# Performance work log

Measured on AMD Instinct MI355X. Metric: run time of the kernel, lower is better.

The kernel has to match this reference:

```python
import jax, jax.numpy as jnp
import numpy as np

E, N, LAT = 200000, 50000, 128
EPS = 1e-8

def _split(x):
    # irreps layout 64x0e | 32x1e | 16x2e, mul-major: [E,64], [E,32,3], [E,16,5]
    n = x.shape[0]
    return x[:, :64], x[:, 64:160].reshape(n, 32, 3), x[:, 160:240].reshape(n, 16, 5)

def _merge(x0, x1, x2):
    n = x0.shape[0]
    return jnp.concatenate([x0, x1.reshape(n, -1), x2.reshape(n, -1)], axis=-1)

def _sep_ln(x, w0, b0, w1, w2):
    # separable layer norm: standard LN on l=0 scalars, degree-balanced RMS on l>0
    x0, x1, x2 = _split(x)
    x0c = x0 - x0.mean(-1, keepdims=True)
    y0 = x0c * jax.lax.rsqrt((x0c * x0c).mean(-1, keepdims=True) + EPS) * w0 + b0
    var = 0.5 * ((x1 * x1).mean((-2, -1)) + (x2 * x2).mean((-2, -1)))
    inv = jax.lax.rsqrt(var + EPS)[:, None, None]
    return _merge(y0, x1 * inv * w1[None, :, None], x2 * inv * w2[None, :, None])

def _rot(x0, x1, x2, D, back=False):
    # per-l Wigner-D block rotation; D is block-diag [E,9,9] (l=0:1x1, l=1:3x3, l=2:5x5)
    sub = 'eji,ecj->eci' if back else 'eij,ecj->eci'
    y0 = x0 * D[:, 0, 0][:, None]
    y1 = jnp.einsum(sub, D[:, 1:4, 1:4], x1)
    y2 = jnp.einsum(sub, D[:, 4:9, 4:9], x2)
    return y0, y1, y2

def _silu(x):
    return x * jax.nn.sigmoid(x)

def _forward(latents, node_features, edge_features, edge_vector, wigner_D_all,
             ln_n_w0, ln_n_b0, ln_n_w1, ln_n_w2, ln_e_w0, ln_e_b0, ln_e_w1, ln_e_w2,
             so2_w0, so2_w1r, so2_w1i, so2_w2r, so2_w2i, lp_w0, lp_b0, lp_w1, lp_w2,
             edge_index, active_edges):
    nn = _sep_ln(node_features, ln_n_w0, ln_n_b0, ln_n_w1, ln_n_w2)
    ne = _sep_ln(edge_features, ln_e_w0, ln_e_b0, ln_e_w1, ln_e_w2)
    ec = edge_index[0][active_edges]
    en = edge_index[1][active_edges]
    lat = latents[active_edges]
    D = wigner_D_all
    # rotate each segment (center | edge | neighbor) into the edge frame (tp_rotate_in)
    segs = [_rot(*_split(s), D) for s in (nn[ec], ne, nn[en])]
    # group by SO(2) order m (index within (2l+1) components is l+m)
    m0 = jnp.concatenate([jnp.concatenate([s0, s1[:, :, 1], s2[:, :, 2]], -1) for s0, s1, s2 in segs] + [lat], -1)  # [E,464]
    p1 = jnp.concatenate([jnp.concatenate([s1[:, :, 2], s2[:, :, 3]], -1) for _, s1, s2 in segs], -1)  # [E,144]
    n1 = jnp.concatenate([jnp.concatenate([s1[:, :, 0], s2[:, :, 1]], -1) for _, s1, s2 in segs], -1)
    p2 = jnp.concatenate([s2[:, :, 4] for _, _, s2 in segs], -1)  # [E,48]
    n2 = jnp.concatenate([s2[:, :, 0] for _, _, s2 in segs], -1)
    # SO(2) linear: real map for m=0 (latents injected), complex 2x2 maps for m>0
    o0 = (m0 @ so2_w0) * (1.0 / np.sqrt(464.0))  # [E,160] = 112 scalars+gates | 32 l1-m0 | 16 l2-m0
    inv1 = 1.0 / np.sqrt(144.0)
    op1 = (p1 @ so2_w1r - n1 @ so2_w1i) * inv1
    on1 = (p1 @ so2_w1i + n1 @ so2_w1r) * inv1
    inv2 = 1.0 / np.sqrt(48.0)
    op2 = (p2 @ so2_w2r - n2 @ so2_w2i) * inv2
    on2 = (p2 @ so2_w2i + n2 @ so2_w2r) * inv2
    s0 = o0[:, :112]
    o1 = jnp.stack([on1[:, :32], o0[:, 112:144], op1[:, :32]], -1)              # [E,32,3]
    o2 = jnp.stack([on2, on1[:, 32:], o0[:, 144:160], op1[:, 32:], op2], -1)   # [E,16,5]
    # rotate back out of the edge frame (tp_rotate_out)
    s0, o1, o2 = _rot(s0, o1, o2, D, back=True)
    # Gate: silu on 64 scalars, sigmoid gates (48) multiply l>0 channels
    gates = jax.nn.sigmoid(s0[:, 64:112])
    sc = _silu(s0[:, :64])
    g1 = o1 * gates[:, :32, None]
    g2 = o2 * gates[:, 32:, None]
    # lin_post: per-l channel-mixing linear, bias on scalars only
    y0 = sc @ lp_w0 * (1.0 / np.sqrt(64.0)) + lp_b0
    y1 = jnp.einsum('ecm,cd->edm', g1, lp_w1) * (1.0 / np.sqrt(32.0))
    y2 = jnp.einsum('ecm,cd->edm', g2, lp_w2) * (1.0 / np.sqrt(16.0))
    return _merge(y0, y1, y2)  # [E,240]

def setup_inputs() -> dict:
    key = jax.random.key(0)
    k = lambda i: jax.random.fold_in(key, i)
    f = lambda i, sh: jax.random.normal(k(i), sh, dtype=jnp.float32)
    return dict(
        latents=f(0, (E, LAT)),
        node_features=f(1, (N, 240)),
        edge_features=f(2, (E, 240)),
        edge_vector=f(3, (E, 3)),
        wigner_D_all=f(4, (E, 9, 9)),
        ln_n_w0=f(5, (64,)), ln_n_b0=f(6, (64,)) * 0.1, ln_n_w1=f(7, (32,)), ln_n_w2=f(8, (16,)),
        ln_e_w0=f(9, (64,)), ln_e_b0=f(10, (64,)) * 0.1, ln_e_w1=f(11, (32,)), ln_e_w2=f(12, (16,)),
        so2_w0=f(13, (464, 160)), so2_w1r=f(14, (144, 48)), so2_w1i=f(15, (144, 48)),
        so2_w2r=f(16, (48, 16)), so2_w2i=f(17, (48, 16)),
        lp_w0=f(18, (64, 64)), lp_b0=f(19, (64,)) * 0.1, lp_w1=f(20, (32, 32)), lp_w2=f(21, (16, 16)),
        edge_index=jax.random.randint(k(22), (2, E), 0, N, dtype=jnp.int32),
        active_edges=jnp.arange(E, dtype=jnp.int32),
    )

def reference(latents, node_features, edge_features, edge_vector, wigner_D_all,
              ln_n_w0, ln_n_b0, ln_n_w1, ln_n_w2, ln_e_w0, ln_e_b0, ln_e_w1, ln_e_w2,
              so2_w0, so2_w1r, so2_w1i, so2_w2r, so2_w2i, lp_w0, lp_b0, lp_w1, lp_w2,
              edge_index, active_edges):
    return _forward(latents, node_features, edge_features, edge_vector, wigner_D_all,
                    ln_n_w0, ln_n_b0, ln_n_w1, ln_n_w2, ln_e_w0, ln_e_b0, ln_e_w1, ln_e_w2,
                    so2_w0, so2_w1r, so2_w1i, so2_w2r, so2_w2i, lp_w0, lp_b0, lp_w1, lp_w2,
                    edge_index, active_edges)
```

## Files before the change

kernel.cpp:

```cpp
#include <hip/hip_runtime.h>
#include <hip/hip_bf16.h>
#include <math.h>

#define NT 512
#define EB 16

using sv4    = __attribute__((ext_vector_type(4))) short;
using short8 = __attribute__((ext_vector_type(8))) short;
using f32x4  = __attribute__((ext_vector_type(4))) float;
using f32x2  = __attribute__((ext_vector_type(2))) float;
typedef unsigned short u16;
typedef unsigned int   u32;

#define MFMA(a,b,c) __builtin_amdgcn_mfma_f32_16x16x32_bf16((a),(b),(c),0,0,0)

#define FW0   0
#define FW1R  150
#define FW1I  165
#define FW1IN 180
#define FW2R  195
#define FW2I  197
#define FW2IN 199
#define FL0   201
#define FL1   209
#define FL2   211
#define NFRAG 212
#define WS_NLS_OFF (NFRAG * 512)

__device__ __forceinline__ u16 f2b(float x) {
  union { float f; u32 u; } v; v.f = x;
  return (u16)((v.u + 0x8000u) >> 16);
}
__device__ __forceinline__ float b2f(u16 u) {
  union { float f; u32 u; } v; v.u = ((u32)u) << 16;
  return v.f;
}
__device__ __forceinline__ sv4 ld4(const u16* p){ return *reinterpret_cast<const sv4*>(p); }

__global__ void prep_w(const float* __restrict__ w0,
                       const float* __restrict__ w1r, const float* __restrict__ w1i,
                       const float* __restrict__ w2r, const float* __restrict__ w2i,
                       const float* __restrict__ l0,  const float* __restrict__ l1,
                       const float* __restrict__ l2,  u16* __restrict__ ws) {
  const int g = blockIdx.x * 256 + threadIdx.x;
  if (g >= NFRAG * 64) return;
  const int frag = g >> 6, lane = g & 63;
  const float* src; int K, N, kt, nt; float sgn = 1.f;
  if (frag < FW1R)       { src = w0;  K = 464; N = 160; int f = frag;       kt = f/10; nt = f%10; }
  else if (frag < FW1I)  { src = w1r; K = 144; N = 48;  int f = frag-FW1R;  kt = f/3;  nt = f%3; }
  else if (frag < FW1IN) { src = w1i; K = 144; N = 48;  int f = frag-FW1I;  kt = f/3;  nt = f%3; }
  else if (frag < FW2R)  { src = w1i; K = 144; N = 48;  int f = frag-FW1IN; kt = f/3;  nt = f%3; sgn = -1.f; }
  else if (frag < FW2I)  { src = w2r; K = 48;  N = 16;  kt = frag-FW2R; nt = 0; }
  else if (frag < FW2IN) { src = w2i; K = 48;  N = 16;  kt = frag-FW2I; nt = 0; }
  else if (frag < FL0)   { src = w2i; K = 48;  N = 16;  kt = frag-FW2IN; nt = 0; sgn = -1.f; }
  else if (frag < FL1)   { src = l0;  K = 64;  N = 64;  int f = frag-FL0;   kt = f/4;  nt = f%4; }
  else if (frag < FL2)   { src = l1;  K = 32;  N = 32;  kt = 0; nt = frag-FL1; }
  else                   { src = l2;  K = 16;  N = 16;  kt = 0; nt = 0; }
  const int n  = nt*16 + (lane & 15);
  const int k0 = kt*32 + (lane >> 4) * 8;
  u16* dst = ws + (size_t)frag * 512 + lane * 8;
  #pragma unroll
  for (int j = 0; j < 8; ++j) {
    const int k = k0 + j;
    const float v = (k < K && n < N) ? src[k * N + n] * sgn : 0.f;
    dst[j] = f2b(v);
  }
}

__global__ void ln_nodes(const float* __restrict__ nodef,
                         const float* __restrict__ w0, const float* __restrict__ b0,
                         const float* __restrict__ w1, const float* __restrict__ w2,
                         u16* __restrict__ nls, int N) {
  const int row  = blockIdx.x * 4 + (threadIdx.x >> 6);
  const int lane = threadIdx.x & 63;
  if (row >= N) return;
  const float* src = nodef + (size_t)row * 240;
  const float v0 = src[lane];
  const float v1 = src[lane + 64];
  const float v2 = src[lane + 128];
  const float v3 = (lane < 48) ? src[lane + 192] : 0.f;
  const bool lo = (lane < 32);
  float sm = v0, sq = v0*v0;
  float S1 = v1*v1 + (lo ? v2*v2 : 0.f);
  float S2 = (lo ? 0.f : v2*v2) + v3*v3;
  #pragma unroll
  for (int s = 32; s > 0; s >>= 1) {
    sm += __shfl_xor(sm, s, 64); sq += __shfl_xor(sq, s, 64);
    S1 += __shfl_xor(S1, s, 64); S2 += __shfl_xor(S2, s, 64);
  }
  const float mu  = sm * (1.f/64.f);
  const float i0  = rsqrtf(sq*(1.f/64.f) - mu*mu + 1e-8f);
  const float inv = rsqrtf(0.5f*(S1*(1.f/96.f) + S2*(1.f/80.f)) + 1e-8f);
  u16* dst = nls + (size_t)row * 320;
  dst[lane] = f2b((v0 - mu) * i0 * w0[lane] + b0[lane]);
  { const int u = lane;      const int c = u/3, j = u-3*c; dst[64 + 4*c + j]  = f2b(v1*inv*w1[c]); }
  if (lo) { const int u = lane+64; const int c = u/3, j = u-3*c; dst[64 + 4*c + j]  = f2b(v2*inv*w1[c]); }
  else    { const int u = lane-32; const int c = u/5, j = u-5*c; dst[192 + 8*c + j] = f2b(v2*inv*w2[c]); }
  if (lane < 48) { const int u = lane+32; const int c = u/5, j = u-5*c; dst[192 + 8*c + j] = f2b(v3*inv*w2[c]); }
  if (lane < 32) dst[64 + 4*lane + 3] = 0;
  if (lane < 48) { const int c = lane/3, j = lane-3*c; dst[192 + 8*c + 5 + j] = 0; }
}

__global__ __launch_bounds__(NT, 4)
void iel_mfma(const float* __restrict__ latents,
              const float* __restrict__ edgef,
              const float* __restrict__ wig,
              const float* __restrict__ ln_e_w0, const float* __restrict__ ln_e_b0,
              const float* __restrict__ ln_e_w1, const float* __restrict__ ln_e_w2,
              const float* __restrict__ lp_b0,
              const int* __restrict__ edge_index, const int* __restrict__ active_edges,
              const u16* __restrict__ ws, const u16* __restrict__ nls,
              float* __restrict__ out,
              int Etot, int A)
{
  __shared__ __align__(16) char SMEM[38848];
  u16*   m0   = (u16*)(SMEM);
  u16*   p1   = (u16*)(SMEM + 15120);
  u16*   n1   = (u16*)(SMEM + 20000);
  u16*   p2   = (u16*)(SMEM + 24880);
  u16*   n2   = (u16*)(SMEM + 26688);
  float* scr  = (float*)(SMEM + 28496);
  float* Dc   = (float*)(SMEM + 36256);
  u16*   g2s  = (u16*)(SMEM + 32336);
  float* o0f  = (float*)(SMEM);
  u16*   g1s  = (u16*)(SMEM + 11008);
  float* op1f = (float*)(SMEM + 15120);
  float* on1f = (float*)(SMEM + 20000);
  float* op2f = (float*)(SMEM + 24880);
  float* on2f = (float*)(SMEM + 26688);
  u16*   gates= (u16*)(SMEM + 28496);
  u16*   scs  = (u16*)(SMEM + 30032);
  float* ot   = (float*)(SMEM + 15120);
  float* yt   = (float*)(SMEM);

  const short8* WF = (const short8*)ws;
  const int t    = threadIdx.x;
  const int lane = t & 63;
  const int w    = t >> 6;
  const int eb0  = blockIdx.x * EB;
  const f32x4 Z4 = {0.f, 0.f, 0.f, 0.f};

  if (t < 256) {
    const int r = t >> 4, c = t & 15;
    if (c < 8) {
      m0[r*472 + 464 + c] = 0;
      p1[r*152 + 144 + c] = 0;
      n1[r*152 + 144 + c] = 0;
      p2[r*56  + 48  + c] = 0;
      n2[r*56  + 48  + c] = 0;
    }
    if (t < 8) {
      m0[16*472 + t] = 0;
      p1[16*152 + t] = 0;
      n1[16*152 + t] = 0;
      p2[16*56  + t] = 0;
      n2[16*56  + t] = 0;
    }
  }

  const int cls = (lane < 32) ? 0 : ((lane < 48) ? 1 : 2);
  const int cc  = (cls == 0) ? lane : (lane & 15);
  const int dbase = (cls == 0) ? 1 : ((cls == 1) ? 12 : 27);
  const int dstr  = (cls == 0) ? 3 : 5;

  const int c1 = lane / 3;
  const bool q2lo = (lane < 32);
  const int c2 = q2lo ? (lane + 64) / 3 : (lane - 32) / 5;
  const int c3 = (lane < 48) ? (lane + 32) / 5 : 15;
  const float w0e = ln_e_w0[lane], b0e = ln_e_b0[lane];
  const float wAe = ln_e_w1[c1];
  const float wBe = q2lo ? ln_e_w1[c2] : ln_e_w2[c2];
  const float wCe = ln_e_w2[c3];

  float* swr = scr + w * 176;

  int aev[2], ecv[2], env[2];
  #pragma unroll
  for (int it = 0; it < 2; ++it) {
    const int e = eb0 + (w<<1) + it;
    aev[it] = active_edges[(e < A) ? e : (A-1)];
  }
  #pragma unroll
  for (int it = 0; it < 2; ++it) {
    ecv[it] = edge_index[aev[it]];
    env[it] = edge_index[Etot + aev[it]];
  }

  #pragma unroll
  for (int it = 0; it < 2; ++it) {
    const int el = (w<<1) + it;
    const int e  = eb0 + el;
    const int eS = (e < A) ? e : (A-1);
    if (lane < 35) {
      int src, dst;
      if (lane == 0)      { src = 0; dst = 0; }
      else if (lane < 10) { const int a=(lane-1)/3, b=(lane-1)-3*((lane-1)/3); src=(1+a)*9+(1+b); dst=lane; }
      else                { const int a=(lane-10)/5, b=(lane-10)-5*((lane-10)/5); src=(4+a)*9+(4+b); dst=lane+2; }
      Dc[el*40 + dst] = wig[(size_t)eS*81 + src];
    } else if (lane < 37) {
      Dc[el*40 + (lane - 25)] = 0.f;
    }
  }

  struct ER {
    u16 q0a, q0b, x4a, x4b;
    sv4 xa, xb;
    float e0, e1, e2, e3, l0, l1;
  };
  ER RA, RB;
  const int xoff = (cls == 0) ? (64 + 4*lane) : (192 + 8*cc);

  auto issue = [&](int it, ER& R) {
    const int e  = eb0 + (w<<1) + it;
    const int eS = (e < A) ? e : (A-1);
    const u16* nba = nls + (size_t)ecv[it]*320;
    const u16* nbb = nls + (size_t)env[it]*320;
    R.q0a = nba[lane]; R.q0b = nbb[lane];
    R.xa = ld4(nba + xoff); R.xb = ld4(nbb + xoff);
    R.x4a = (cls == 0) ? (u16)0 : nba[xoff + 4];
    R.x4b = (cls == 0) ? (u16)0 : nbb[xoff + 4];
    const float* ep = edgef + (size_t)eS*240;
    R.e0 = ep[lane]; R.e1 = ep[lane+64]; R.e2 = ep[lane+128];
    R.e3 = (lane < 48) ? ep[lane+192] : 0.f;
    const float* lr = latents + (size_t)aev[it]*128;
    R.l0 = lr[lane]; R.l1 = lr[64+lane];
  };

  auto process = [&](int it, ER& R) {
    const int el = (w<<1) + it;
    const float* DcE = Dc + el*40;
    const float d00 = DcE[0];
    float d[3][5];
    #pragma unroll
    for (int i = 0; i < 3; ++i)
      #pragma unroll
      for (int j = 0; j < 5; ++j)
        d[i][j] = DcE[dbase + i*dstr + j];

    u16* B0; u16* B1; u16* B2; int S0, S1, S2;
    if (cls == 0)      { B0 = n1 + el*152 + cc;      S0 = 48;  B1 = m0 + el*472 + 64 + cc; S1 = 112; B2 = p1 + el*152 + cc;      S2 = 48; }
    else if (cls == 1) { B0 = n2 + el*56  + cc;      S0 = 16;  B1 = n1 + el*152 + 32 + cc; S1 = 48;  B2 = m0 + el*472 + 96 + cc; S2 = 112; }
    else               { B0 = p1 + el*152 + 32 + cc; S0 = 48;  B1 = p2 + el*56  + cc;      S1 = 16;  B2 = m0;                    S2 = 0; }

    {
      f32x2 x0 = {b2f((u16)R.xa[0]), b2f((u16)R.xb[0])};
      f32x2 x1 = {b2f((u16)R.xa[1]), b2f((u16)R.xb[1])};
      f32x2 x2 = {b2f((u16)R.xa[2]), b2f((u16)R.xb[2])};
      f32x2 x3 = {b2f((u16)R.xa[3]), b2f((u16)R.xb[3])};
      f32x2 x4 = {b2f(R.x4a), b2f(R.x4b)};
      f32x2 q0 = {b2f(R.q0a), b2f(R.q0b)};
      f32x2 q0d = q0 * d00;
      m0[el*472 + lane]       = f2b(q0d[0]);
      m0[el*472 + 224 + lane] = f2b(q0d[1]);
      f32x2 s0 = x0*d[0][0] + x1*d[0][1] + x2*d[0][2] + x3*d[0][3] + x4*d[0][4];
      f32x2 s1 = x0*d[1][0] + x1*d[1][1] + x2*d[1][2] + x3*d[1][3] + x4*d[1][4];
      f32x2 s2 = x0*d[2][0] + x1*d[2][1] + x2*d[2][2] + x3*d[2][3] + x4*d[2][4];
      B0[0] = f2b(s0[0]); B0[2*S0] = f2b(s0[1]);
      B1[0] = f2b(s1[0]); B1[2*S1] = f2b(s1[1]);
      if (lane < 48) { B2[0] = f2b(s2[0]); B2[2*S2] = f2b(s2[1]); }
    }

    {
      const float v0 = R.e0, v1 = R.e1, v2 = R.e2, v3 = R.e3;
      float sm = v0, sq = v0*v0;
      float S1r = v1*v1 + (q2lo ? v2*v2 : 0.f);
      float S2r = (q2lo ? 0.f : v2*v2) + v3*v3;
      #pragma unroll
      for (int s = 32; s > 0; s >>= 1) {
        sm += __shfl_xor(sm, s, 64);  sq += __shfl_xor(sq, s, 64);
        S1r += __shfl_xor(S1r, s, 64); S2r += __shfl_xor(S2r, s, 64);
      }
      const float mu = sm * (1.f/64.f);
      const float i0 = rsqrtf(sq*(1.f/64.f) - mu*mu + 1e-8f);
      const float iv = rsqrtf(0.5f*(S1r*(1.f/96.f) + S2r*(1.f/80.f)) + 1e-8f);
      swr[lane]      = v1 * iv * wAe;
      swr[64 + lane] = v2 * iv * wBe;
      if (lane < 48) swr[128 + lane] = v3 * iv * wCe;
      asm volatile("s_waitcnt lgkmcnt(0)" ::: "memory");
      m0[el*472 + 112 + lane] = f2b(((v0 - mu)*i0*w0e + b0e) * d00);
      const float* sb = (cls == 0) ? (swr + 3*cc) : (swr + 96 + 5*cc);
      const float x0 = sb[0], x1 = sb[1], x2 = sb[2];
      const float x3 = (cls == 0) ? 0.f : sb[3];
      const float x4 = (cls == 0) ? 0.f : sb[4];
      float s0v = d[0][0]*x0 + d[0][1]*x1 + d[0][2]*x2 + d[0][3]*x3 + d[0][4]*x4;
      float s1v = d[1][0]*x0 + d[1][1]*x1 + d[1][2]*x2 + d[1][3]*x3 + d[1][4]*x4;
      float s2v = d[2][0]*x0 + d[2][1]*x1 + d[2][2]*x2 + d[2][3]*x3 + d[2][4]*x4;
      B0[S0] = f2b(s0v);
      B1[S1] = f2b(s1v);
      if (lane < 48) B2[S2] = f2b(s2v);
    }
    m0[el*472 + 336 + lane] = f2b(R.l0);
    m0[el*472 + 400 + lane] = f2b(R.l1);
  };

  issue(0, RA);
  issue(1, RB);
  process(0, RA);
  process(1, RB);
  __syncthreads();

  f32x4 acc2a[2] = {Z4, Z4};
  {
    const u16* abase = m0 + (lane & 15)*472 + (lane >> 4)*8;
    #pragma unroll
    for (int kt = 0; kt < 15; ++kt) {
      const short8 a = *reinterpret_cast<const short8*>(abase + kt*32);
      acc2a[0] = MFMA(a, WF[(size_t)(FW0 + kt*10 + w)*64 + lane], acc2a[0]);
      if (w < 2)
        acc2a[1] = MFMA(a, WF[(size_t)(FW0 + kt*10 + 8 + w)*64 + lane], acc2a[1]);
    }
  }
  f32x4 acc2b = Z4;
  f32x4 acc2c = Z4;
  if (w < 6) {
    const u16* pbase = p1 + (lane & 15)*152 + (lane >> 4)*8;
    const u16* nbase = n1 + (lane & 15)*152 + (lane >> 4)*8;
    const int isOn = (w >= 3) ? 1 : 0;
    const int nt2 = w - 3*isOn;
    #pragma unroll
    for (int kt = 0; kt < 5; ++kt) {
      const short8 pa = *reinterpret_cast<const short8*>(pbase + kt*32);
      const short8 na = *reinterpret_cast<const short8*>(nbase + kt*32);
      acc2b = MFMA(pa, WF[(size_t)((isOn?FW1I:FW1R)  + kt*3 + nt2)*64 + lane], acc2b);
      acc2b = MFMA(na, WF[(size_t)((isOn?FW1R:FW1IN) + kt*3 + nt2)*64 + lane], acc2b);
    }
  } else {
    const u16* pb2 = p2 + (lane & 15)*56 + (lane >> 4)*8;
    const u16* nb2 = n2 + (lane & 15)*56 + (lane >> 4)*8;
    const int isOn2 = (w == 7);
    #pragma unroll
    for (int kt = 0; kt < 2; ++kt) {
      const short8 pa = *reinterpret_cast<const short8*>(pb2 + kt*32);
      const short8 na = *reinterpret_cast<const short8*>(nb2 + kt*32);
      acc2c = MFMA(pa, WF[(size_t)((isOn2?FW2I:FW2R)  + kt)*64 + lane], acc2c);
      acc2c = MFMA(na, WF[(size_t)((isOn2?FW2R:FW2IN) + kt)*64 + lane], acc2c);
    }
  }
  __syncthreads();

  {
    const int col = w*16 + (lane & 15);
    const int r0  = (lane >> 4)*4;
    #pragma unroll
    for (int j = 0; j < 4; ++j)
      o0f[(r0+j)*172 + col] = acc2a[0][j] * 0.046423835f;
    if (w < 2) {
      const int col2 = (8+w)*16 + (lane & 15);
      #pragma unroll
      for (int j = 0; j < 4; ++j)
        o0f[(r0+j)*172 + col2] = acc2a[1][j] * 0.046423835f;
    }
  }
  __syncthreads();

  {
    if (w < 6) {
      const int isOn = (w >= 3) ? 1 : 0;
      const int nt2 = w - 3*isOn;
      float* dst = isOn ? on1f : op1f;
      const int col = nt2*16 + (lane & 15);
      const int r0  = (lane >> 4)*4;
      #pragma unroll
      for (int j = 0; j < 4; ++j)
        dst[(r0+j)*52 + col] = acc2b[j] * (1.f/12.f);
    } else {
      float* dst = (w == 7) ? on2f : op2f;
      const int r0 = (lane >> 4)*4;
      #pragma unroll
      for (int j = 0; j < 4; ++j)
        dst[(r0+j)*20 + (lane & 15)] = acc2c[j] * 0.14433757f;
    }
  }
  {
    const int e = t >> 5, l32 = t & 31;
    const float d0 = Dc[e*40];
    #pragma unroll
    for (int k = 0; k < 4; ++k) {
      const int p = l32 + 32*k;
      if (p < 112) {
        const float x = o0f[e*172 + p] * d0;
        const float sg = 1.f/(1.f + __expf(-x));
        if (p < 64) scs[e*72 + p] = f2b(x * sg);
        else        gates[e*48 + (p - 64)] = f2b(sg);
      }
    }
  }
  if (t < 256) {
    const int r = t >> 4, c = t & 15;
    if (c < 8) {
      #pragma unroll
      for (int m = 0; m < 5; ++m) g2s[m*392 + r*24 + 16 + c] = 0;
    }
    if (t < 8) {
      #pragma unroll
      for (int m = 0; m < 5; ++m) g2s[m*392 + 384 + t] = 0;
    }
  }
  __syncthreads();

  {
    const int e = t >> 5, l32 = t & 31;
    const float* DcE = Dc + e*40;
    #pragma unroll
    for (int k = 0; k < 3; ++k) {
      const int item = l32 + 32*k;
      const int c = item/3, m = item - 3*c;
      const float val = DcE[1 + m]     * on1f[e*52 + c]
                      + DcE[1 + 3 + m] * o0f[e*172 + 112 + c]
                      + DcE[1 + 6 + m] * op1f[e*52 + c];
      const float g = b2f(gates[e*48 + c]);
      g1s[m*640 + e*40 + c] = f2b(val * g);
    }
    if (l32 < 16) {
      const int c = l32;
      const float f0 = on2f[e*20 + c];
      const float f1 = on1f[e*52 + 32 + c];
      const float f2c = o0f[e*172 + 144 + c];
      const float f3 = op1f[e*52 + 32 + c];
      const float f4 = op2f[e*20 + c];
      const float gg = b2f(gates[e*48 + 32 + c]);
      #pragma unroll
      for (int m = 0; m < 5; ++m) {
        const float val = DcE[12 + m]*f0 + DcE[12 + 5 + m]*f1 + DcE[12 + 10 + m]*f2c
                        + DcE[12 + 15 + m]*f3 + DcE[12 + 20 + m]*f4;
        g2s[m*392 + e*24 + c] = f2b(val * gg);
      }
    }
  }
  __syncthreads();

  for (int tau = w; tau < 15; tau += 8) {
    const int col16 = lane & 15;
    const int r0 = (lane >> 4)*4;
    if (tau < 4) {
      const int ntt = tau;
      f32x4 a0 = Z4;
      #pragma unroll
      for (int kt = 0; kt < 2; ++kt) {
        const short8 a = *reinterpret_cast<const short8*>(
            scs + (lane & 15)*72 + kt*32 + (lane >> 4)*8);
        a0 = MFMA(a, WF[(size_t)(FL0 + kt*4 + ntt)*64 + lane], a0);
      }
      const int col = ntt*16 + col16;
      const float bias = lp_b0[col];
      #pragma unroll
      for (int j = 0; j < 4; ++j)
        yt[(r0+j)*64 + col] = a0[j]*0.125f + bias;
    } else if (tau < 10) {
      const int u = tau - 4, m = u >> 1, ntt = u & 1;
      const short8 a = *reinterpret_cast<const short8*>(
          g1s + m*640 + (lane & 15)*40 + (lane >> 4)*8);
      f32x4 a0 = Z4;
      a0 = MFMA(a, WF[(size_t)(FL1 + ntt)*64 + lane], a0);
      const int oc = (ntt*16 + col16)*3 + m;
      #pragma unroll
      for (int j = 0; j < 4; ++j)
        ot[(r0+j)*176 + oc] = a0[j]*0.17677670f;
    } else {
      const int m = tau - 10;
      const short8 a = *reinterpret_cast<const short8*>(
          g2s + m*392 + (lane & 15)*24 + (lane >> 4)*8);
      f32x4 a0 = Z4;
      a0 = MFMA(a, WF[(size_t)FL2*64 + lane], a0);
      const int oc = 96 + col16*5 + m;
      #pragma unroll
      for (int j = 0; j < 4; ++j)
        ot[(r0+j)*176 + oc] = a0[j]*0.25f;
    }
  }
  __syncthreads();

  for (int idx = t; idx < 16*60; idx += NT) {
    const int row = idx / 60, seg = idx - row*60;
    const int er = eb0 + row;
    if (er < A) {
      f32x4 v;
      if (seg < 16) v = *reinterpret_cast<const f32x4*>(yt + row*64 + seg*4);
      else          v = *reinterpret_cast<const f32x4*>(ot + row*176 + (seg-16)*4);
      *reinterpret_cast<f32x4*>(out + (size_t)er*240 + seg*4) = v;
    }
  }
}

extern "C" void kernel_launch(void* const* d_in, const int* in_sizes, int n_in,
                              void* d_out, int out_size, void* d_ws, size_t ws_size,
                              hipStream_t stream) {
  const float* latents  = (const float*)d_in[0];
  const float* nodef    = (const float*)d_in[1];
  const float* edgef    = (const float*)d_in[2];
  const float* wig      = (const float*)d_in[4];
  const float* ln_n_w0  = (const float*)d_in[5];
  const float* ln_n_b0  = (const float*)d_in[6];
  const float* ln_n_w1  = (const float*)d_in[7];
  const float* ln_n_w2  = (const float*)d_in[8];
  const float* ln_e_w0  = (const float*)d_in[9];
  const float* ln_e_b0  = (const float*)d_in[10];
  const float* ln_e_w1  = (const float*)d_in[11];
  const float* ln_e_w2  = (const float*)d_in[12];
  const float* so2_w0   = (const float*)d_in[13];
  const float* so2_w1r  = (const float*)d_in[14];
  const float* so2_w1i  = (const float*)d_in[15];
  const float* so2_w2r  = (const float*)d_in[16];
  const float* so2_w2i  = (const float*)d_in[17];
  const float* lp_w0    = (const float*)d_in[18];
  const float* lp_b0    = (const float*)d_in[19];
  const float* lp_w1    = (const float*)d_in[20];
  const float* lp_w2    = (const float*)d_in[21];
  const int*   edge_index   = (const int*)d_in[22];
  const int*   active_edges = (const int*)d_in[23];

  const int Etot = in_sizes[2] / 240;
  const int N    = in_sizes[1] / 240;
  const int A    = in_sizes[23];

  u16* ws  = (u16*)d_ws;
  u16* nls = ws + WS_NLS_OFF;

  const int pthreads = NFRAG * 64;
  hipLaunchKernelGGL(prep_w, dim3((pthreads + 255) / 256), dim3(256), 0, stream,
                     so2_w0, so2_w1r, so2_w1i, so2_w2r, so2_w2i,
                     lp_w0, lp_w1, lp_w2, ws);

  hipLaunchKernelGGL(ln_nodes, dim3((N + 3) / 4), dim3(256), 0, stream,
                     nodef, ln_n_w0, ln_n_b0, ln_n_w1, ln_n_w2, nls, N);

  const int grid = (A + EB - 1) / EB;
  hipLaunchKernelGGL(iel_mfma, dim3(grid), dim3(NT), 0, stream,
                     latents, edgef, wig,
                     ln_e_w0, ln_e_b0, ln_e_w1, ln_e_w2,
                     lp_b0, edge_index, active_edges, ws, nls,
                     (float*)d_out, Etot, A);
}
```

Before: 345.9 us.

## Precompute edge layer norm into bf16 table and rebalance MFMA work across waves

Adds an optional pre-pass that applies the separable layer norm to edge features and stores them as a padded bf16 table, so the main kernel reads a smaller per-edge row instead of fp32 features plus an in-kernel reduction. The path is taken only when the workspace is large enough. The extra m0 output tiles move from waves 0-1 to waves 6-7, which do less SO(2) work, to balance MFMA load. The two store phases merge so one barrier is dropped. The pre-pass costs a separate launch that reads and writes all edges, and the edge data is now rounded to bf16 before rotation.

```diff
diff --git a/kernel.cpp b/kernel.cpp
--- a/kernel.cpp
+++ b/kernel.cpp
@@ -25,7 +25,7 @@
 #define FL1   209
 #define FL2   211
 #define NFRAG 212
-#define WS_NLS_OFF (NFRAG * 512)
+#define WS_NLS_OFF ((size_t)NFRAG * 512)
 
 __device__ __forceinline__ u16 f2b(float x) {
   union { float f; u32 u; } v; v.f = x;
@@ -67,14 +67,14 @@
   }
 }
 
-__global__ void ln_nodes(const float* __restrict__ nodef,
-                         const float* __restrict__ w0, const float* __restrict__ b0,
-                         const float* __restrict__ w1, const float* __restrict__ w2,
-                         u16* __restrict__ nls, int N) {
+__global__ void ln_rows(const float* __restrict__ rows,
+                        const float* __restrict__ w0, const float* __restrict__ b0,
+                        const float* __restrict__ w1, const float* __restrict__ w2,
+                        u16* __restrict__ tab, int R) {
   const int row  = blockIdx.x * 4 + (threadIdx.x >> 6);
   const int lane = threadIdx.x & 63;
-  if (row >= N) return;
-  const float* src = nodef + (size_t)row * 240;
+  if (row >= R) return;
+  const float* src = rows + (size_t)row * 240;
   const float v0 = src[lane];
   const float v1 = src[lane + 64];
   const float v2 = src[lane + 128];
@@ -91,7 +91,7 @@
   const float mu  = sm * (1.f/64.f);
   const float i0  = rsqrtf(sq*(1.f/64.f) - mu*mu + 1e-8f);
   const float inv = rsqrtf(0.5f*(S1*(1.f/96.f) + S2*(1.f/80.f)) + 1e-8f);
-  u16* dst = nls + (size_t)row * 320;
+  u16* dst = tab + (size_t)row * 320;
   dst[lane] = f2b((v0 - mu) * i0 * w0[lane] + b0[lane]);
   { const int u = lane;      const int c = u/3, j = u-3*c; dst[64 + 4*c + j]  = f2b(v1*inv*w1[c]); }
   if (lo) { const int u = lane+64; const int c = u/3, j = u-3*c; dst[64 + 4*c + j]  = f2b(v2*inv*w1[c]); }
@@ -101,6 +101,7 @@
   if (lane < 48) { const int c = lane/3, j = lane-3*c; dst[192 + 8*c + 5 + j] = 0; }
 }
 
+template<int PRE>
 __global__ __launch_bounds__(NT, 4)
 void iel_mfma(const float* __restrict__ latents,
               const float* __restrict__ edgef,
@@ -110,6 +111,7 @@
               const float* __restrict__ lp_b0,
               const int* __restrict__ edge_index, const int* __restrict__ active_edges,
               const u16* __restrict__ ws, const u16* __restrict__ nls,
+              const u16* __restrict__ els,
               float* __restrict__ out,
               int Etot, int A)
 {
@@ -167,11 +169,13 @@
   const bool q2lo = (lane < 32);
   const int c2 = q2lo ? (lane + 64) / 3 : (lane - 32) / 5;
   const int c3 = (lane < 48) ? (lane + 32) / 5 : 15;
-  const float w0e = ln_e_w0[lane], b0e = ln_e_b0[lane];
-  const float wAe = ln_e_w1[c1];
-  const float wBe = q2lo ? ln_e_w1[c2] : ln_e_w2[c2];
-  const float wCe = ln_e_w2[c3];
-
+  float w0e = 0.f, b0e = 0.f, wAe = 0.f, wBe = 0.f, wCe = 0.f;
+  if (!PRE) {
+    w0e = ln_e_w0[lane]; b0e = ln_e_b0[lane];
+    wAe = ln_e_w1[c1];
+    wBe = q2lo ? ln_e_w1[c2] : ln_e_w2[c2];
+    wCe = ln_e_w2[c3];
+  }
   float* swr = scr + w * 176;
 
   int aev[2], ecv[2], env[2];
@@ -203,8 +207,8 @@
   }
 
   struct ER {
-    u16 q0a, q0b, x4a, x4b;
-    sv4 xa, xb;
+    u16 q0a, q0b, q0e, x4a, x4b, x4e;
+    sv4 xa, xb, xe;
     float e0, e1, e2, e3, l0, l1;
   };
   ER RA, RB;
@@ -219,9 +223,16 @@
     R.xa = ld4(nba + xoff); R.xb = ld4(nbb + xoff);
     R.x4a = (cls == 0) ? (u16)0 : nba[xoff + 4];
     R.x4b = (cls == 0) ? (u16)0 : nbb[xoff + 4];
-    const float* ep = edgef + (size_t)eS*240;
-    R.e0 = ep[lane]; R.e1 = ep[lane+64]; R.e2 = ep[lane+128];
-    R.e3 = (lane < 48) ? ep[lane+192] : 0.f;
+    if (PRE) {
+      const u16* ebp = els + (size_t)eS*320;
+      R.q0e = ebp[lane];
+      R.xe  = ld4(ebp + xoff);
+      R.x4e = (cls == 0) ? (u16)0 : ebp[xoff + 4];
+    } else {
+      const float* ep = edgef + (size_t)eS*240;
+      R.e0 = ep[lane]; R.e1 = ep[lane+64]; R.e2 = ep[lane+128];
+      R.e3 = (lane < 48) ? ep[lane+192] : 0.f;
+    }
     const float* lr = latents + (size_t)aev[it]*128;
     R.l0 = lr[lane]; R.l1 = lr[64+lane];
   };
@@ -260,7 +271,18 @@
       if (lane < 48) { B2[0] = f2b(s2[0]); B2[2*S2] = f2b(s2[1]); }
     }
 
-    {
+    if (PRE) {
+      m0[el*472 + 112 + lane] = f2b(b2f(R.q0e) * d00);
+      const float x0 = b2f((u16)R.xe[0]), x1 = b2f((u16)R.xe[1]);
+      const float x2 = b2f((u16)R.xe[2]), x3 = b2f((u16)R.xe[3]);
+      const float x4 = b2f(R.x4e);
+      float s0v = d[0][0]*x0 + d[0][1]*x1 + d[0][2]*x2 + d[0][3]*x3 + d[0][4]*x4;
+      float s1v = d[1][0]*x0 + d[1][1]*x1 + d[1][2]*x2 + d[1][3]*x3 + d[1][4]*x4;
+      float s2v = d[2][0]*x0 + d[2][1]*x1 + d[2][2]*x2 + d[2][3]*x3 + d[2][4]*x4;
+      B0[S0] = f2b(s0v);
+      B1[S1] = f2b(s1v);
+      if (lane < 48) B2[S2] = f2b(s2v);
+    } else {
       const float v0 = R.e0, v1 = R.e1, v2 = R.e2, v3 = R.e3;
       float sm = v0, sq = v0*v0;
       float S1r = v1*v1 + (q2lo ? v2*v2 : 0.f);
@@ -306,8 +328,8 @@
     for (int kt = 0; kt < 15; ++kt) {
       const short8 a = *reinterpret_cast<const short8*>(abase + kt*32);
       acc2a[0] = MFMA(a, WF[(size_t)(FW0 + kt*10 + w)*64 + lane], acc2a[0]);
-      if (w < 2)
-        acc2a[1] = MFMA(a, WF[(size_t)(FW0 + kt*10 + 8 + w)*64 + lane], acc2a[1]);
+      if (w >= 6)
+        acc2a[1] = MFMA(a, WF[(size_t)(FW0 + kt*10 + (w+2))*64 + lane], acc2a[1]);
     }
   }
   f32x4 acc2b = Z4;
@@ -344,33 +366,29 @@
     #pragma unroll
     for (int j = 0; j < 4; ++j)
       o0f[(r0+j)*172 + col] = acc2a[0][j] * 0.046423835f;
-    if (w < 2) {
-      const int col2 = (8+w)*16 + (lane & 15);
+    if (w >= 6) {
+      const int col2 = (w+2)*16 + (lane & 15);
       #pragma unroll
       for (int j = 0; j < 4; ++j)
         o0f[(r0+j)*172 + col2] = acc2a[1][j] * 0.046423835f;
     }
-  }
-  __syncthreads();
-
-  {
     if (w < 6) {
       const int isOn = (w >= 3) ? 1 : 0;
       const int nt2 = w - 3*isOn;
       float* dst = isOn ? on1f : op1f;
-      const int col = nt2*16 + (lane & 15);
-      const int r0  = (lane >> 4)*4;
+      const int colb = nt2*16 + (lane & 15);
       #pragma unroll
       for (int j = 0; j < 4; ++j)
-        dst[(r0+j)*52 + col] = acc2b[j] * (1.f/12.f);
+        dst[(r0+j)*52 + colb] = acc2b[j] * (1.f/12.f);
     } else {
       float* dst = (w == 7) ? on2f : op2f;
-      const int r0 = (lane >> 4)*4;
       #pragma unroll
       for (int j = 0; j < 4; ++j)
         dst[(r0+j)*20 + (lane & 15)] = acc2c[j] * 0.14433757f;
     }
   }
+  __syncthreads();
+
   {
     const int e = t >> 5, l32 = t & 31;
     const float d0 = Dc[e*40];
@@ -515,19 +533,35 @@
 
   u16* ws  = (u16*)d_ws;
   u16* nls = ws + WS_NLS_OFF;
+  u16* els = nls + (size_t)N * 320;
+  const size_t need = (WS_NLS_OFF + (size_t)N*320 + (size_t)Etot*320) * 2;
+  const bool pre = (ws_size >= need);
 
   const int pthreads = NFRAG * 64;
   hipLaunchKernelGGL(prep_w, dim3((pthreads + 255) / 256), dim3(256), 0, stream,
                      so2_w0, so2_w1r, so2_w1i, so2_w2r, so2_w2i,
                      lp_w0, lp_w1, lp_w2, ws);
 
-  hipLaunchKernelGGL(ln_nodes, dim3((N + 3) / 4), dim3(256), 0, stream,
+  hipLaunchKernelGGL(ln_rows, dim3((N + 3) / 4), dim3(256), 0, stream,
                      nodef, ln_n_w0, ln_n_b0, ln_n_w1, ln_n_w2, nls, N);
 
+  if (pre) {
+    hipLaunchKernelGGL(ln_rows, dim3((Etot + 3) / 4), dim3(256), 0, stream,
+                       edgef, ln_e_w0, ln_e_b0, ln_e_w1, ln_e_w2, els, Etot);
+  }
+
   const int grid = (A + EB - 1) / EB;
-  hipLaunchKernelGGL(iel_mfma, dim3(grid), dim3(NT), 0, stream,
-                     latents, edgef, wig,
-                     ln_e_w0, ln_e_b0, ln_e_w1, ln_e_w2,
-                     lp_b0, edge_index, active_edges, ws, nls,
-                     (float*)d_out, Etot, A);
+  if (pre) {
+    hipLaunchKernelGGL((iel_mfma<1>), dim3(grid), dim3(NT), 0, stream,
+                       latents, edgef, wig,
+                       ln_e_w0, ln_e_b0, ln_e_w1, ln_e_w2,
+                       lp_b0, edge_index, active_edges, ws, nls, els,
+                       (float*)d_out, Etot, A);
+  } else {
+    hipLaunchKernelGGL((iel_mfma<0>), dim3(grid), dim3(NT), 0, stream,
+                       latents, edgef, wig,
+                       ln_e_w0, ln_e_b0, ln_e_w1, ln_e_w2,
+                       lp_b0, edge_index, active_edges, ws, nls, nls,
+                       (float*)d_out, Etot, A);
+  }
 }
```

Result: slower. 419.7 us (+21.3%).
